# Performance work log

Measured on AMD Instinct MI355X. Metric: run time of the kernel, lower is better.

The kernel has to match this reference:

```python
import jax, jax.numpy as jnp
import numpy as np

B, N, E, H = 8, 512, 256, 8
DK = E // H
DIST_BAR = (0.3, 0.7, 1e10)  # init dist_bar + [1e10] appended in forward
NEG = -1e10


def setup_inputs() -> dict:
    key = jax.random.key(0)
    ks = jax.random.split(key, 24)
    s = 0.02
    inp = {
        'query': jax.random.normal(ks[0], (B, N, E), jnp.float32),
        'key':   jax.random.normal(ks[1], (B, N, E), jnp.float32),
        'value': jax.random.normal(ks[2], (B, N, E), jnp.float32),
        'dist':  jax.random.uniform(ks[3], (B, N, N), jnp.float32),
        'mask':  jax.random.randint(ks[4], (B, N, N), 0, 2).astype(jnp.int32),
        # 4 linears (q, k, v, out), stored as [in, out] for x @ W
        'Wq': jax.random.normal(ks[5], (E, E)) * s, 'bq': jnp.zeros((E,)),
        'Wk': jax.random.normal(ks[6], (E, E)) * s, 'bk': jnp.zeros((E,)),
        'Wv': jax.random.normal(ks[7], (E, E)) * s, 'bv': jnp.zeros((E,)),
        'Wo': jax.random.normal(ks[8], (E, E)) * s, 'bo': jnp.zeros((E,)),
        # cnn: Conv2d(1,H,1) -> ReLU -> Conv2d(H,H,1); 1x1 convs = per-pixel linear maps
        'cw1': jax.random.normal(ks[9], (H,)) * s,     'cb1': jnp.zeros((H,)),
        'cw2': jax.random.normal(ks[10], (H, H)) * s,  'cb2': jnp.zeros((H,)),
        # scale_linear: Linear(3E, E) -> ReLU -> Linear(E, E)
        'Ws1': jax.random.normal(ks[11], (3 * E, E)) * s, 'bs1': jnp.zeros((E,)),
        'Ws2': jax.random.normal(ks[12], (E, E)) * s,     'bs2': jnp.zeros((E,)),
    }
    return inp


def reference(query, key, value, dist, mask,
              Wq, bq, Wk, bk, Wv, bv, Wo, bo,
              cw1, cb1, cw2, cb2, Ws1, bs1, Ws2, bs2):
    def heads(x, W, b):  # [B,N,E] -> [B,H,N,DK]
        return (x @ W + b).reshape(B, N, H, DK).transpose(0, 2, 1, 3)

    q, k, v = heads(query, Wq, bq), heads(key, Wk, bk), heads(value, Wv, bv)
    d4 = dist[:, None]  # [B,1,N,N]
    # 1x1 conv stack: [B,1,N,N] -> [B,H,N,N]
    c1 = jax.nn.relu(d4 * cw1[None, :, None, None] + cb1[None, :, None, None])
    dist_conv = jnp.einsum('oi,bijk->bojk', cw2, c1) + cb2[None, :, None, None]

    scores = jnp.einsum('bhqd,bhkd->bhqk', q, k) / np.sqrt(DK).astype(np.float32)
    scores = scores * dist_conv
    scores = jnp.where(mask[:, None] == 0, NEG, scores)

    outs = []
    for bar in DIST_BAR:
        dm = d4 < bar                       # [B,1,N,N] bool
        dm = dm.at[:, :, 0, :].set(True).at[:, :, :, 0].set(True)
        s = jnp.where(dm, scores, NEG)
        p = jax.nn.softmax(s, axis=-1)      # [B,H,N,N]
        o = jnp.einsum('bhqk,bhkd->bhqd', p, v)
        o = o.transpose(0, 2, 1, 3).reshape(B, N, E)
        outs.append(o @ Wo + bo)
    x = jnp.concatenate(outs, axis=-1)      # [B,N,3E]
    h1 = jax.nn.relu(x @ Ws1 + bs1)
    return h1 @ Ws2 + bs2                   # [B,N,E]
```

## Files before the change

kernel.cpp:

```cpp
#include <hip/hip_runtime.h>
#include <math.h>

typedef _Float16 h16;
typedef __attribute__((ext_vector_type(8))) _Float16 h16x8;
typedef __attribute__((ext_vector_type(4))) float f32x4;
typedef unsigned long long u64t;
typedef unsigned int u32t;
typedef unsigned short u16t;
typedef unsigned char u8t;

__global__ void bcomb_k(const float* __restrict__ bo, const float* __restrict__ Ws1,
                        const float* __restrict__ bs1, float* __restrict__ bcomb)
{
    const int jj = threadIdx.x;
    const int r0 = blockIdx.x * 64;
    float acc = (blockIdx.x == 0) ? bs1[jj] : 0.f;
    for (int r = r0; r < r0 + 64; ++r)
        acc = fmaf(bo[r & 255], Ws1[(size_t)r * 256 + jj], acc);
    atomicAdd(&bcomb[jj], acc);
}

__global__ __launch_bounds__(256) void transpose_k(
    const float* __restrict__ Wq, const float* __restrict__ Wk,
    const float* __restrict__ Wv, const float* __restrict__ Ws2,
    const float* __restrict__ Ws1, h16* __restrict__ WT)
{
    const int z = blockIdx.z;
    const float* in = (z == 0) ? Wq : (z == 1) ? Wk : (z == 2) ? Wv :
                      (z == 3) ? Ws2 : (Ws1 + (size_t)(z - 4) * 65536);
    h16* out = WT + (size_t)z * 65536;
    __shared__ float T[32][33];
    const int t = threadIdx.x, tx = t & 31, ty = t >> 5;
    const int r0 = blockIdx.x * 32, c0 = blockIdx.y * 32;
    #pragma unroll
    for (int i = 0; i < 4; ++i) {
        const int row = ty + i * 8;
        T[row][tx] = in[(size_t)(r0 + row) * 256 + c0 + tx];
    }
    __syncthreads();
    #pragma unroll
    for (int i = 0; i < 4; ++i) {
        const int row = ty + i * 8;
        out[(size_t)(c0 + row) * 256 + r0 + tx] = (h16)T[tx][row];
    }
}

template<int A_F32, int MODE>
__global__ __launch_bounds__(256) void hgemm_k(
    const void* __restrict__ Av, const h16* __restrict__ Bt0,
    const float* __restrict__ bias, void* __restrict__ outv,
    int M, int Nn, int K, long btz, int ldt)
{
    const h16* Bt = Bt0 + (size_t)blockIdx.z * btz;
    __shared__ __align__(16) h16 As[64][40];
    __shared__ __align__(16) h16 Bs[64][40];
    const int t = threadIdx.x, w = t >> 6, lane = t & 63;
    const int Q = lane >> 4, n = lane & 15;
    const int row0 = blockIdx.x * 64, col0 = blockIdx.y * 64;
    const int sr = t >> 2, sc = (t & 3) * 8;
    f32x4 acc[4];
    #pragma unroll
    for (int c = 0; c < 4; ++c) acc[c] = (f32x4){0.f, 0.f, 0.f, 0.f};

    for (int k0 = 0; k0 < K; k0 += 32) {
        __syncthreads();
        if (A_F32) {
            const float* ap = (const float*)Av + (size_t)(row0 + sr) * K + k0 + sc;
            float4 f0 = *(const float4*)ap;
            float4 f1 = *(const float4*)(ap + 4);
            h16x8 hv;
            hv[0] = (h16)f0.x; hv[1] = (h16)f0.y; hv[2] = (h16)f0.z; hv[3] = (h16)f0.w;
            hv[4] = (h16)f1.x; hv[5] = (h16)f1.y; hv[6] = (h16)f1.z; hv[7] = (h16)f1.w;
            *(h16x8*)&As[sr][sc] = hv;
        } else {
            *(h16x8*)&As[sr][sc] =
                *(const h16x8*)((const h16*)Av + (size_t)(row0 + sr) * K + k0 + sc);
        }
        *(h16x8*)&Bs[sr][sc] = *(const h16x8*)(Bt + (size_t)(col0 + sr) * K + k0 + sc);
        __syncthreads();
        h16x8 af = *(const h16x8*)&As[w * 16 + n][Q * 8];
        #pragma unroll
        for (int c = 0; c < 4; ++c) {
            h16x8 bf = *(const h16x8*)&Bs[c * 16 + n][Q * 8];
            acc[c] = __builtin_amdgcn_mfma_f32_16x16x32_f16(af, bf, acc[c], 0, 0, 0);
        }
    }

    float bvv[4] = {0.f, 0.f, 0.f, 0.f};
    if (MODE != 4) {
        #pragma unroll
        for (int c = 0; c < 4; ++c) bvv[c] = bias[col0 + c * 16 + n];
    }
    #pragma unroll
    for (int c = 0; c < 4; ++c) {
        #pragma unroll
        for (int r = 0; r < 4; ++r) {
            const int row = row0 + w * 16 + 4 * Q + r;
            const int col = col0 + c * 16 + n;
            if (MODE == 0) {
                ((float*)outv)[(size_t)row * Nn + col] = acc[c][r] + bvv[c];
            } else if (MODE == 2) {
                ((h16*)outv)[(size_t)row * Nn + col] = (h16)fmaxf(acc[c][r] + bvv[c], 0.f);
            } else {
                ((h16*)outv)[(size_t)col * ldt + (int)blockIdx.z * M + row] = (h16)acc[c][r];
            }
        }
    }
}

__global__ __launch_bounds__(256) void qkv_hgemm_k(
    const float* __restrict__ Xq, const float* __restrict__ Xk,
    const float* __restrict__ Xv, const h16* __restrict__ WT,
    const float* __restrict__ bq, const float* __restrict__ bk,
    const float* __restrict__ bv,
    h16* __restrict__ qb, h16* __restrict__ kb, h16* __restrict__ vbT)
{
    const int z = blockIdx.z;
    const float* A    = (z == 0) ? Xq : (z == 1) ? Xk : Xv;
    const h16*   Bt   = WT + (size_t)z * 65536;
    const float* bias = (z == 0) ? bq : (z == 1) ? bk : bv;

    __shared__ __align__(16) h16 As[64][40];
    __shared__ __align__(16) h16 Bs[64][40];
    const int t = threadIdx.x, w = t >> 6, lane = t & 63;
    const int Q = lane >> 4, n = lane & 15;
    const int row0 = blockIdx.x * 64, col0 = blockIdx.y * 64;
    const int sr = t >> 2, sc = (t & 3) * 8;
    f32x4 acc[4];
    #pragma unroll
    for (int c = 0; c < 4; ++c) acc[c] = (f32x4){0.f, 0.f, 0.f, 0.f};

    for (int k0 = 0; k0 < 256; k0 += 32) {
        __syncthreads();
        {
            const float* ap = A + (size_t)(row0 + sr) * 256 + k0 + sc;
            float4 f0 = *(const float4*)ap;
            float4 f1 = *(const float4*)(ap + 4);
            h16x8 hv;
            hv[0] = (h16)f0.x; hv[1] = (h16)f0.y; hv[2] = (h16)f0.z; hv[3] = (h16)f0.w;
            hv[4] = (h16)f1.x; hv[5] = (h16)f1.y; hv[6] = (h16)f1.z; hv[7] = (h16)f1.w;
            *(h16x8*)&As[sr][sc] = hv;
            *(h16x8*)&Bs[sr][sc] = *(const h16x8*)(Bt + (size_t)(col0 + sr) * 256 + k0 + sc);
        }
        __syncthreads();
        h16x8 af = *(const h16x8*)&As[w * 16 + n][Q * 8];
        #pragma unroll
        for (int c = 0; c < 4; ++c) {
            h16x8 bf = *(const h16x8*)&Bs[c * 16 + n][Q * 8];
            acc[c] = __builtin_amdgcn_mfma_f32_16x16x32_f16(af, bf, acc[c], 0, 0, 0);
        }
    }

    float bvv[4];
    #pragma unroll
    for (int c = 0; c < 4; ++c) bvv[c] = bias[col0 + c * 16 + n];

    if (z < 2) {
        h16* out = z ? kb : qb;
        #pragma unroll
        for (int c = 0; c < 4; ++c)
            #pragma unroll
            for (int r = 0; r < 4; ++r)
                out[(size_t)(row0 + w * 16 + 4 * Q + r) * 256 + col0 + c * 16 + n] =
                    (h16)(acc[c][r] + bvv[c]);
    } else {
        const int bb = row0 >> 9;
        #pragma unroll
        for (int c = 0; c < 4; ++c)
            #pragma unroll
            for (int r = 0; r < 4; ++r) {
                const int m = row0 + w * 16 + 4 * Q + r;
                const int col = col0 + c * 16 + n;
                vbT[((size_t)(bb * 256 + col)) * 512 + (m & 511)] = (h16)(acc[c][r] + bvv[c]);
            }
    }
}

__global__ __launch_bounds__(256, 4) void attn_k(
    const h16* __restrict__ qb, const h16* __restrict__ kb,
    const h16* __restrict__ vbT,
    const float* __restrict__ dist, const int* __restrict__ mask,
    const float* __restrict__ cw1, const float* __restrict__ cb1,
    const float* __restrict__ cw2, const float* __restrict__ cb2,
    h16* __restrict__ OB)
{
    const int bx = blockIdx.x, b = bx >> 5, q0 = (bx & 31) * 16;
    const int t = threadIdx.x, w = t >> 6, lane = t & 63;
    const int Q = lane >> 4, n = lane & 15;
    const int h = blockIdx.y * 4 + w;

    __shared__ __align__(16) h16 c1t[16][65][8];
    __shared__ __align__(16) u8t Cd[16][72];
    __shared__ __align__(16) h16 Sx[4][16][72];

    const float invs = 0.17677669529663687f;
    float w1[8], b1[8], w2w[8];
    #pragma unroll
    for (int u = 0; u < 8; ++u) {
        w1[u] = cw1[u]; b1[u] = cb1[u];
        w2w[u] = invs * cw2[h * 8 + u];
    }
    const float fb = invs * cb2[h];

    const h16x8 aq =
        *(const h16x8*)(qb + ((size_t)(b * 512 + q0 + n)) * 256 + h * 32 + Q * 8);

    const f32x4 z4 = {0.f, 0.f, 0.f, 0.f};
    f32x4 acc[3][2];
    #pragma unroll
    for (int s = 0; s < 3; ++s) { acc[s][0] = z4; acc[s][1] = z4; }
    float mprev = -3e38f;
    float lsum[3] = {0.f, 0.f, 0.f};

    const int scol = t & 63, srow0 = t >> 6;

    for (int kc = 0; kc < 8; ++kc) {
        const int kk0 = kc * 64;
        __syncthreads();
        #pragma unroll
        for (int i = 0; i < 4; ++i) {
            const int row = srow0 + 4 * i;
            const size_t off = ((size_t)(b * 512 + q0 + row)) * 512 + kk0 + scol;
            const float d = dist[off];
            const int mk = mask[off];
            const bool fr = ((q0 + row) == 0) || ((kk0 + scol) == 0);
            const bool keep = (mk != 0);
            const u32t code = (keep && (fr || d < 0.3f) ? 1u : 0u)
                            | (keep && (fr || d < 0.7f) ? 2u : 0u)
                            | (keep ? 4u : 0u);
            Cd[row][scol] = (u8t)code;
            h16x8 ch;
            #pragma unroll
            for (int u = 0; u < 8; ++u)
                ch[u] = (h16)fmaxf(fmaf(d, w1[u], b1[u]), 0.f);
            *(h16x8*)&c1t[row][scol][0] = ch;
        }
        __syncthreads();

        f32x4 s4[4];
        #pragma unroll
        for (int cg = 0; cg < 4; ++cg) {
            h16x8 kf = *(const h16x8*)(
                kb + ((size_t)(b * 512 + kk0 + cg * 16 + n)) * 256 + h * 32 + Q * 8);
            s4[cg] = __builtin_amdgcn_mfma_f32_16x16x32_f16(aq, kf, z4, 0, 0, 0);
        }
        #pragma unroll
        for (int cg = 0; cg < 4; ++cg) {
            #pragma unroll
            for (int r = 0; r < 4; ++r) {
                h16x8 ch = *(const h16x8*)&c1t[4 * Q + r][cg * 16 + n][0];
                float f = fb;
                #pragma unroll
                for (int u = 0; u < 8; ++u)
                    f = fmaf((float)ch[u], w2w[u], f);
                Sx[w][4 * Q + r][cg * 16 + n] = (h16)(s4[cg][r] * f);
            }
        }
        __builtin_amdgcn_wave_barrier();

        float sv[16];
        u64t cd0 = *(const u64t*)&Cd[n][Q * 8];
        u64t cd1 = *(const u64t*)&Cd[n][32 + Q * 8];
        {
            h16x8 sh0 = *(const h16x8*)&Sx[w][n][Q * 8];
            h16x8 sh1 = *(const h16x8*)&Sx[w][n][32 + Q * 8];
            #pragma unroll
            for (int j = 0; j < 8; ++j) { sv[j] = (float)sh0[j]; sv[8 + j] = (float)sh1[j]; }
        }
        float cm = -3e38f;
        #pragma unroll
        for (int i = 0; i < 16; ++i) {
            const u32t cc = (u32t)((i < 8 ? cd0 : cd1) >> (8 * (i & 7))) & 7u;
            cm = fmaxf(cm, (cc & 4u) ? sv[i] : -3e38f);
        }
        cm = fmaxf(cm, __shfl_xor(cm, 16));
        cm = fmaxf(cm, __shfl_xor(cm, 32));
        const float mnew = fmaxf(mprev, cm);
        const float alphaA = __expf(mprev - mnew);
        mprev = mnew;

        #pragma unroll
        for (int r = 0; r < 4; ++r) {
            const float aR = __shfl(alphaA, 4 * Q + r);
            #pragma unroll
            for (int s = 0; s < 3; ++s) { acc[s][0][r] *= aR; acc[s][1][r] *= aR; }
        }

        h16x8 pf[3][2];
        float l0 = 0.f, l1 = 0.f, l2 = 0.f;
        #pragma unroll
        for (int i = 0; i < 16; ++i) {
            const u32t cc = (u32t)((i < 8 ? cd0 : cd1) >> (8 * (i & 7))) & 7u;
            const float e = __expf(sv[i] - mnew);
            const float p0 = (cc & 1u) ? e : 0.f;
            const float p1 = (cc & 2u) ? e : 0.f;
            const float p2 = (cc & 4u) ? e : 0.f;
            l0 += p0; l1 += p1; l2 += p2;
            pf[0][i >> 3][i & 7] = (h16)p0;
            pf[1][i >> 3][i & 7] = (h16)p1;
            pf[2][i >> 3][i & 7] = (h16)p2;
        }
        lsum[0] = lsum[0] * alphaA + l0;
        lsum[1] = lsum[1] * alphaA + l1;
        lsum[2] = lsum[2] * alphaA + l2;

        #pragma unroll
        for (int kb2 = 0; kb2 < 2; ++kb2) {
            #pragma unroll
            for (int nh = 0; nh < 2; ++nh) {
                h16x8 vf = *(const h16x8*)(
                    vbT + ((size_t)((b * 8 + h) * 32 + nh * 16 + n)) * 512
                        + kk0 + kb2 * 32 + Q * 8);
                #pragma unroll
                for (int s = 0; s < 3; ++s)
                    acc[s][nh] = __builtin_amdgcn_mfma_f32_16x16x32_f16(
                        pf[s][kb2], vf, acc[s][nh], 0, 0, 0);
            }
        }
    }

    float lrow[3];
    #pragma unroll
    for (int s = 0; s < 3; ++s) {
        float lv = lsum[s];
        lv += __shfl_xor(lv, 16);
        lv += __shfl_xor(lv, 32);
        lrow[s] = lv;
    }
    #pragma unroll
    for (int s = 0; s < 3; ++s) {
        #pragma unroll
        for (int r = 0; r < 4; ++r) {
            const float il = 1.0f / __shfl(lrow[s], 4 * Q + r);
            const size_t row = (size_t)(b * 512 + q0 + 4 * Q + r);
            h16* op = OB + row * 768 + s * 256 + h * 32 + n;
            op[0]  = (h16)(acc[s][0][r] * il);
            op[16] = (h16)(acc[s][1][r] * il);
        }
    }
}

extern "C" void kernel_launch(void* const* d_in, const int* in_sizes, int n_in,
                              void* d_out, int out_size, void* d_ws, size_t ws_size,
                              hipStream_t stream)
{
    const float* query = (const float*)d_in[0];
    const float* key   = (const float*)d_in[1];
    const float* value = (const float*)d_in[2];
    const float* dist  = (const float*)d_in[3];
    const int*   mask  = (const int*)d_in[4];
    const float* Wq = (const float*)d_in[5];  const float* bq = (const float*)d_in[6];
    const float* Wk = (const float*)d_in[7];  const float* bk = (const float*)d_in[8];
    const float* Wv = (const float*)d_in[9];  const float* bv = (const float*)d_in[10];
    const float* Wo = (const float*)d_in[11]; const float* bo = (const float*)d_in[12];
    const float* cw1 = (const float*)d_in[13]; const float* cb1 = (const float*)d_in[14];
    const float* cw2 = (const float*)d_in[15]; const float* cb2 = (const float*)d_in[16];
    const float* Ws1 = (const float*)d_in[17]; const float* bs1 = (const float*)d_in[18];
    const float* Ws2 = (const float*)d_in[19]; const float* bs2 = (const float*)d_in[20];

    h16* qb    = (h16*)d_ws;
    h16* kb    = qb + 1048576;
    h16* vbT   = kb + 1048576;
    h16* OB    = vbT + 1048576;
    h16* h1    = OB + 3145728;
    h16* WT    = h1 + 1048576;
    h16* WbigT = WT + 458752;
    float* bcomb = (float*)(WbigT + 196608);

    hipMemsetAsync(bcomb, 0, 256 * sizeof(float), stream);
    bcomb_k<<<dim3(12), dim3(256), 0, stream>>>(bo, Ws1, bs1, bcomb);

    transpose_k<<<dim3(8, 8, 7), 256, 0, stream>>>(Wq, Wk, Wv, Ws2, Ws1, WT);

    hgemm_k<1, 4><<<dim3(4, 4, 3), 256, 0, stream>>>(
        Wo, WT + 4 * 65536, nullptr, WbigT, 256, 256, 256, 65536, 768);

    qkv_hgemm_k<<<dim3(64, 4, 3), 256, 0, stream>>>(
        query, key, value, WT, bq, bk, bv, qb, kb, vbT);

    attn_k<<<dim3(256, 2), 256, 0, stream>>>(
        qb, kb, vbT, dist, mask, cw1, cb1, cw2, cb2, OB);

    hgemm_k<0, 2><<<dim3(64, 4, 1), 256, 0, stream>>>(
        OB, WbigT, bcomb, h1, 4096, 256, 768, 0, 0);
    hgemm_k<0, 0><<<dim3(64, 4, 1), 256, 0, stream>>>(
        h1, WT + 3 * 65536, bs2, d_out, 4096, 256, 256, 0, 0);
}
```

Baseline: 193.2 us.

## Fuse prep kernels, double-buffer GEMMs and prefetch attention tiles

Merges the weight-transpose and bias-combination kernels into one launch and folds the Wo weight-combination GEMM into the QKV projection launch, which drops the memset and several launches. All GEMMs now double-buffer shared memory with register prefetch, and the tail GEMMs use 32-row tiles with K-step 64 so they launch more blocks. Attention precomputes the per-head conv factor during staging and prefetches the next chunk's dist/mask/K/V into registers. It lowers attention occupancy to 2 blocks per SM to make room for the extra registers.

```diff
diff --git a/kernel.cpp b/kernel.cpp
--- a/kernel.cpp
+++ b/kernel.cpp
@@ -6,177 +6,225 @@
 typedef __attribute__((ext_vector_type(4))) float f32x4;
 typedef unsigned long long u64t;
 typedef unsigned int u32t;
-typedef unsigned short u16t;
 typedef unsigned char u8t;
 
-__global__ void bcomb_k(const float* __restrict__ bo, const float* __restrict__ Ws1,
-                        const float* __restrict__ bs1, float* __restrict__ bcomb)
-{
-    const int jj = threadIdx.x;
-    const int r0 = blockIdx.x * 64;
-    float acc = (blockIdx.x == 0) ? bs1[jj] : 0.f;
-    for (int r = r0; r < r0 + 64; ++r)
-        acc = fmaf(bo[r & 255], Ws1[(size_t)r * 256 + jj], acc);
-    atomicAdd(&bcomb[jj], acc);
-}
-
-__global__ __launch_bounds__(256) void transpose_k(
+__global__ __launch_bounds__(256) void prep_k(
     const float* __restrict__ Wq, const float* __restrict__ Wk,
     const float* __restrict__ Wv, const float* __restrict__ Ws2,
-    const float* __restrict__ Ws1, h16* __restrict__ WT)
+    const float* __restrict__ Ws1, const float* __restrict__ bo,
+    const float* __restrict__ bs1, h16* __restrict__ WT,
+    float* __restrict__ bcomb)
 {
-    const int z = blockIdx.z;
-    const float* in = (z == 0) ? Wq : (z == 1) ? Wk : (z == 2) ? Wv :
-                      (z == 3) ? Ws2 : (Ws1 + (size_t)(z - 4) * 65536);
-    h16* out = WT + (size_t)z * 65536;
+    const int bid = blockIdx.x;
     __shared__ float T[32][33];
-    const int t = threadIdx.x, tx = t & 31, ty = t >> 5;
-    const int r0 = blockIdx.x * 32, c0 = blockIdx.y * 32;
-    #pragma unroll
-    for (int i = 0; i < 4; ++i) {
-        const int row = ty + i * 8;
-        T[row][tx] = in[(size_t)(r0 + row) * 256 + c0 + tx];
-    }
-    __syncthreads();
-    #pragma unroll
-    for (int i = 0; i < 4; ++i) {
-        const int row = ty + i * 8;
-        out[(size_t)(c0 + row) * 256 + r0 + tx] = (h16)T[tx][row];
+    if (bid < 448) {
+        const int z = bid >> 6, idx = bid & 63;
+        const float* in = (z == 0) ? Wq : (z == 1) ? Wk : (z == 2) ? Wv :
+                          (z == 3) ? Ws2 : (Ws1 + (size_t)(z - 4) * 65536);
+        h16* out = WT + (size_t)z * 65536;
+        const int t = threadIdx.x, tx = t & 31, ty = t >> 5;
+        const int r0 = (idx >> 3) * 32, c0 = (idx & 7) * 32;
+        #pragma unroll
+        for (int i = 0; i < 4; ++i)
+            T[ty + i * 8][tx] = in[(size_t)(r0 + ty + i * 8) * 256 + c0 + tx];
+        __syncthreads();
+        #pragma unroll
+        for (int i = 0; i < 4; ++i)
+            out[(size_t)(c0 + ty + i * 8) * 256 + r0 + tx] = (h16)T[tx][ty + i * 8];
+    } else {
+        const int j = threadIdx.x;
+        float acc = bs1[j];
+        for (int r = 0; r < 768; ++r)
+            acc = fmaf(bo[r & 255], Ws1[(size_t)r * 256 + j], acc);
+        bcomb[j] = acc;
     }
 }
 
-template<int A_F32, int MODE>
-__global__ __launch_bounds__(256) void hgemm_k(
-    const void* __restrict__ Av, const h16* __restrict__ Bt0,
-    const float* __restrict__ bias, void* __restrict__ outv,
-    int M, int Nn, int K, long btz, int ldt)
+__global__ __launch_bounds__(256) void qkvw_k(
+    const float* __restrict__ Xq, const float* __restrict__ Xk,
+    const float* __restrict__ Xv, const float* __restrict__ Wo,
+    const h16* __restrict__ WT,
+    const float* __restrict__ bq, const float* __restrict__ bk,
+    const float* __restrict__ bv,
+    h16* __restrict__ qb, h16* __restrict__ kb, h16* __restrict__ vbT,
+    h16* __restrict__ WbigT)
 {
-    const h16* Bt = Bt0 + (size_t)blockIdx.z * btz;
-    __shared__ __align__(16) h16 As[64][40];
-    __shared__ __align__(16) h16 Bs[64][40];
+    const int bid = blockIdx.x;
+    const float* A; const h16* Bt; const float* bias = nullptr;
+    int mode, row0, col0, sgm = 0;
+    if (bid < 768) {
+        const int z = bid >> 8, r = bid & 255;
+        row0 = (r & 63) * 64; col0 = (r >> 6) * 64;
+        A = (z == 0) ? Xq : (z == 1) ? Xk : Xv;
+        Bt = WT + (size_t)z * 65536;
+        bias = (z == 0) ? bq : (z == 1) ? bk : bv;
+        mode = z;
+    } else {
+        const int r = bid - 768;
+        sgm = r >> 4; const int tt = r & 15;
+        row0 = (tt >> 2) * 64; col0 = (tt & 3) * 64;
+        A = Wo; Bt = WT + (size_t)(4 + sgm) * 65536; mode = 3;
+    }
+
+    __shared__ __align__(16) h16 As[2][64][40];
+    __shared__ __align__(16) h16 Bs[2][64][40];
     const int t = threadIdx.x, w = t >> 6, lane = t & 63;
     const int Q = lane >> 4, n = lane & 15;
-    const int row0 = blockIdx.x * 64, col0 = blockIdx.y * 64;
     const int sr = t >> 2, sc = (t & 3) * 8;
-    f32x4 acc[4];
-    #pragma unroll
-    for (int c = 0; c < 4; ++c) acc[c] = (f32x4){0.f, 0.f, 0.f, 0.f};
-
-    for (int k0 = 0; k0 < K; k0 += 32) {
+
+    auto ldA = [&](int k0) -> h16x8 {
+        const float* ap = A + (size_t)(row0 + sr) * 256 + k0 + sc;
+        float4 f0 = *(const float4*)ap;
+        float4 f1 = *(const float4*)(ap + 4);
+        h16x8 hv;
+        hv[0] = (h16)f0.x; hv[1] = (h16)f0.y; hv[2] = (h16)f0.z; hv[3] = (h16)f0.w;
+        hv[4] = (h16)f1.x; hv[5] = (h16)f1.y; hv[6] = (h16)f1.z; hv[7] = (h16)f1.w;
+        return hv;
+    };
+    auto ldB = [&](int k0) -> h16x8 {
+        return *(const h16x8*)(Bt + (size_t)(col0 + sr) * 256 + k0 + sc);
+    };
+
+    {
+        h16x8 a0 = ldA(0), b0 = ldB(0);
+        *(h16x8*)&As[0][sr][sc] = a0;
+        *(h16x8*)&Bs[0][sr][sc] = b0;
+    }
+    __syncthreads();
+
+    f32x4 acc4[4];
+    #pragma unroll
+    for (int c = 0; c < 4; ++c) acc4[c] = (f32x4){0.f, 0.f, 0.f, 0.f};
+
+    for (int it = 0; it < 8; ++it) {
+        const int cur = it & 1;
+        h16x8 arN, brN;
+        if (it < 7) { arN = ldA(32 * (it + 1)); brN = ldB(32 * (it + 1)); }
+        h16x8 af = *(const h16x8*)&As[cur][w * 16 + n][Q * 8];
+        #pragma unroll
+        for (int cg = 0; cg < 4; ++cg) {
+            h16x8 bf = *(const h16x8*)&Bs[cur][cg * 16 + n][Q * 8];
+            acc4[cg] = __builtin_amdgcn_mfma_f32_16x16x32_f16(af, bf, acc4[cg], 0, 0, 0);
+        }
+        if (it < 7) {
+            *(h16x8*)&As[cur ^ 1][sr][sc] = arN;
+            *(h16x8*)&Bs[cur ^ 1][sr][sc] = brN;
+        }
         __syncthreads();
-        if (A_F32) {
-            const float* ap = (const float*)Av + (size_t)(row0 + sr) * K + k0 + sc;
-            float4 f0 = *(const float4*)ap;
-            float4 f1 = *(const float4*)(ap + 4);
-            h16x8 hv;
-            hv[0] = (h16)f0.x; hv[1] = (h16)f0.y; hv[2] = (h16)f0.z; hv[3] = (h16)f0.w;
-            hv[4] = (h16)f1.x; hv[5] = (h16)f1.y; hv[6] = (h16)f1.z; hv[7] = (h16)f1.w;
-            *(h16x8*)&As[sr][sc] = hv;
-        } else {
-            *(h16x8*)&As[sr][sc] =
-                *(const h16x8*)((const h16*)Av + (size_t)(row0 + sr) * K + k0 + sc);
-        }
-        *(h16x8*)&Bs[sr][sc] = *(const h16x8*)(Bt + (size_t)(col0 + sr) * K + k0 + sc);
-        __syncthreads();
-        h16x8 af = *(const h16x8*)&As[w * 16 + n][Q * 8];
-        #pragma unroll
-        for (int c = 0; c < 4; ++c) {
-            h16x8 bf = *(const h16x8*)&Bs[c * 16 + n][Q * 8];
-            acc[c] = __builtin_amdgcn_mfma_f32_16x16x32_f16(af, bf, acc[c], 0, 0, 0);
-        }
-    }
-
-    float bvv[4] = {0.f, 0.f, 0.f, 0.f};
-    if (MODE != 4) {
-        #pragma unroll
-        for (int c = 0; c < 4; ++c) bvv[c] = bias[col0 + c * 16 + n];
-    }
-    #pragma unroll
-    for (int c = 0; c < 4; ++c) {
-        #pragma unroll
-        for (int r = 0; r < 4; ++r) {
-            const int row = row0 + w * 16 + 4 * Q + r;
-            const int col = col0 + c * 16 + n;
-            if (MODE == 0) {
-                ((float*)outv)[(size_t)row * Nn + col] = acc[c][r] + bvv[c];
-            } else if (MODE == 2) {
-                ((h16*)outv)[(size_t)row * Nn + col] = (h16)fmaxf(acc[c][r] + bvv[c], 0.f);
-            } else {
-                ((h16*)outv)[(size_t)col * ldt + (int)blockIdx.z * M + row] = (h16)acc[c][r];
+    }
+
+    if (mode < 2) {
+        h16* out = mode ? kb : qb;
+        #pragma unroll
+        for (int cg = 0; cg < 4; ++cg) {
+            const float bvv = bias[col0 + cg * 16 + n];
+            #pragma unroll
+            for (int r = 0; r < 4; ++r)
+                out[(size_t)(row0 + w * 16 + 4 * Q + r) * 256 + col0 + cg * 16 + n] =
+                    (h16)(acc4[cg][r] + bvv);
+        }
+    } else if (mode == 2) {
+        const int bb = row0 >> 9;
+        #pragma unroll
+        for (int cg = 0; cg < 4; ++cg) {
+            const float bvv = bias[col0 + cg * 16 + n];
+            const int col = col0 + cg * 16 + n;
+            #pragma unroll
+            for (int r = 0; r < 4; ++r) {
+                const int m = row0 + w * 16 + 4 * Q + r;
+                vbT[((size_t)(bb * 256 + col)) * 512 + (m & 511)] = (h16)(acc4[cg][r] + bvv);
             }
         }
+    } else {
+        #pragma unroll
+        for (int cg = 0; cg < 4; ++cg) {
+            const int col = col0 + cg * 16 + n;
+            #pragma unroll
+            for (int r = 0; r < 4; ++r)
+                WbigT[(size_t)col * 768 + sgm * 256 + row0 + w * 16 + 4 * Q + r] =
+                    (h16)acc4[cg][r];
+        }
     }
 }
 
-__global__ __launch_bounds__(256) void qkv_hgemm_k(
-    const float* __restrict__ Xq, const float* __restrict__ Xk,
-    const float* __restrict__ Xv, const h16* __restrict__ WT,
-    const float* __restrict__ bq, const float* __restrict__ bk,
-    const float* __restrict__ bv,
-    h16* __restrict__ qb, h16* __restrict__ kb, h16* __restrict__ vbT)
+template<int OUT16RELU>
+__global__ __launch_bounds__(256) void hgemm32_k(
+    const h16* __restrict__ A, const h16* __restrict__ Bt,
+    const float* __restrict__ bias, void* __restrict__ outv, int K)
 {
-    const int z = blockIdx.z;
-    const float* A    = (z == 0) ? Xq : (z == 1) ? Xk : Xv;
-    const h16*   Bt   = WT + (size_t)z * 65536;
-    const float* bias = (z == 0) ? bq : (z == 1) ? bk : bv;
-
-    __shared__ __align__(16) h16 As[64][40];
-    __shared__ __align__(16) h16 Bs[64][40];
+    __shared__ __align__(16) h16 As[2][32][72];
+    __shared__ __align__(16) h16 Bs[2][64][72];
     const int t = threadIdx.x, w = t >> 6, lane = t & 63;
     const int Q = lane >> 4, n = lane & 15;
-    const int row0 = blockIdx.x * 64, col0 = blockIdx.y * 64;
-    const int sr = t >> 2, sc = (t & 3) * 8;
-    f32x4 acc[4];
-    #pragma unroll
-    for (int c = 0; c < 4; ++c) acc[c] = (f32x4){0.f, 0.f, 0.f, 0.f};
-
-    for (int k0 = 0; k0 < 256; k0 += 32) {
+    const int row0 = blockIdx.x * 32, col0 = blockIdx.y * 64;
+    const int r16 = (w & 1) * 16, c32 = (w >> 1) * 32;
+    const int asr = t >> 3, asc = (t & 7) * 8;
+    const int bsr = t >> 2, bsc = (t & 3) * 16;
+
+    auto ldA = [&](int k0) -> h16x8 {
+        return *(const h16x8*)(A + (size_t)(row0 + asr) * K + k0 + asc);
+    };
+    auto ldB0 = [&](int k0) -> h16x8 {
+        return *(const h16x8*)(Bt + (size_t)(col0 + bsr) * K + k0 + bsc);
+    };
+    auto ldB1 = [&](int k0) -> h16x8 {
+        return *(const h16x8*)(Bt + (size_t)(col0 + bsr) * K + k0 + bsc + 8);
+    };
+
+    {
+        h16x8 a0 = ldA(0), b0 = ldB0(0), b1 = ldB1(0);
+        *(h16x8*)&As[0][asr][asc] = a0;
+        *(h16x8*)&Bs[0][bsr][bsc] = b0;
+        *(h16x8*)&Bs[0][bsr][bsc + 8] = b1;
+    }
+    __syncthreads();
+
+    f32x4 acc2[2];
+    acc2[0] = (f32x4){0.f, 0.f, 0.f, 0.f};
+    acc2[1] = (f32x4){0.f, 0.f, 0.f, 0.f};
+    const int iters = K >> 6;
+
+    for (int it = 0; it < iters; ++it) {
+        const int cur = it & 1;
+        h16x8 arN, brN0, brN1;
+        if (it + 1 < iters) {
+            arN = ldA(64 * (it + 1));
+            brN0 = ldB0(64 * (it + 1));
+            brN1 = ldB1(64 * (it + 1));
+        }
+        #pragma unroll
+        for (int kh = 0; kh < 2; ++kh) {
+            h16x8 af = *(const h16x8*)&As[cur][r16 + n][kh * 32 + Q * 8];
+            #pragma unroll
+            for (int cg = 0; cg < 2; ++cg) {
+                h16x8 bf = *(const h16x8*)&Bs[cur][c32 + cg * 16 + n][kh * 32 + Q * 8];
+                acc2[cg] = __builtin_amdgcn_mfma_f32_16x16x32_f16(af, bf, acc2[cg], 0, 0, 0);
+            }
+        }
+        if (it + 1 < iters) {
+            *(h16x8*)&As[cur ^ 1][asr][asc] = arN;
+            *(h16x8*)&Bs[cur ^ 1][bsr][bsc] = brN0;
+            *(h16x8*)&Bs[cur ^ 1][bsr][bsc + 8] = brN1;
+        }
         __syncthreads();
-        {
-            const float* ap = A + (size_t)(row0 + sr) * 256 + k0 + sc;
-            float4 f0 = *(const float4*)ap;
-            float4 f1 = *(const float4*)(ap + 4);
-            h16x8 hv;
-            hv[0] = (h16)f0.x; hv[1] = (h16)f0.y; hv[2] = (h16)f0.z; hv[3] = (h16)f0.w;
-            hv[4] = (h16)f1.x; hv[5] = (h16)f1.y; hv[6] = (h16)f1.z; hv[7] = (h16)f1.w;
-            *(h16x8*)&As[sr][sc] = hv;
-            *(h16x8*)&Bs[sr][sc] = *(const h16x8*)(Bt + (size_t)(col0 + sr) * 256 + k0 + sc);
-        }
-        __syncthreads();
-        h16x8 af = *(const h16x8*)&As[w * 16 + n][Q * 8];
-        #pragma unroll
-        for (int c = 0; c < 4; ++c) {
-            h16x8 bf = *(const h16x8*)&Bs[c * 16 + n][Q * 8];
-            acc[c] = __builtin_amdgcn_mfma_f32_16x16x32_f16(af, bf, acc[c], 0, 0, 0);
-        }
-    }
-
-    float bvv[4];
-    #pragma unroll
-    for (int c = 0; c < 4; ++c) bvv[c] = bias[col0 + c * 16 + n];
-
-    if (z < 2) {
-        h16* out = z ? kb : qb;
-        #pragma unroll
-        for (int c = 0; c < 4; ++c)
-            #pragma unroll
-            for (int r = 0; r < 4; ++r)
-                out[(size_t)(row0 + w * 16 + 4 * Q + r) * 256 + col0 + c * 16 + n] =
-                    (h16)(acc[c][r] + bvv[c]);
-    } else {
-        const int bb = row0 >> 9;
-        #pragma unroll
-        for (int c = 0; c < 4; ++c)
-            #pragma unroll
-            for (int r = 0; r < 4; ++r) {
-                const int m = row0 + w * 16 + 4 * Q + r;
-                const int col = col0 + c * 16 + n;
-                vbT[((size_t)(bb * 256 + col)) * 512 + (m & 511)] = (h16)(acc[c][r] + bvv[c]);
-            }
+    }
+
+    #pragma unroll
+    for (int cg = 0; cg < 2; ++cg) {
+        const int col = col0 + c32 + cg * 16 + n;
+        const float bv = bias[col];
+        #pragma unroll
+        for (int r = 0; r < 4; ++r) {
+            const int row = row0 + r16 + 4 * Q + r;
+            if (OUT16RELU)
+                ((h16*)outv)[(size_t)row * 256 + col] = (h16)fmaxf(acc2[cg][r] + bv, 0.f);
+            else
+                ((float*)outv)[(size_t)row * 256 + col] = acc2[cg][r] + bv;
+        }
     }
 }
 
-__global__ __launch_bounds__(256, 4) void attn_k(
+__global__ __launch_bounds__(256, 2) void attn_k(
     const h16* __restrict__ qb, const h16* __restrict__ kb,
     const h16* __restrict__ vbT,
     const float* __restrict__ dist, const int* __restrict__ mask,
@@ -185,22 +233,26 @@
     h16* __restrict__ OB)
 {
     const int bx = blockIdx.x, b = bx >> 5, q0 = (bx & 31) * 16;
+    const int hg = blockIdx.y;
     const int t = threadIdx.x, w = t >> 6, lane = t & 63;
     const int Q = lane >> 4, n = lane & 15;
-    const int h = blockIdx.y * 4 + w;
-
-    __shared__ __align__(16) h16 c1t[16][65][8];
-    __shared__ __align__(16) u8t Cd[16][72];
+    const int h = hg * 4 + w;
+
+    __shared__ __align__(16) h16 Ft[2][4][16][68];
+    __shared__ __align__(16) u8t Cd[2][16][72];
     __shared__ __align__(16) h16 Sx[4][16][72];
 
     const float invs = 0.17677669529663687f;
-    float w1[8], b1[8], w2w[8];
-    #pragma unroll
-    for (int u = 0; u < 8; ++u) {
-        w1[u] = cw1[u]; b1[u] = cb1[u];
-        w2w[u] = invs * cw2[h * 8 + u];
-    }
-    const float fb = invs * cb2[h];
+    float w1[8], b1[8];
+    #pragma unroll
+    for (int u = 0; u < 8; ++u) { w1[u] = cw1[u]; b1[u] = cb1[u]; }
+    float w2a[4][8], fba[4];
+    #pragma unroll
+    for (int hh = 0; hh < 4; ++hh) {
+        #pragma unroll
+        for (int u = 0; u < 8; ++u) w2a[hh][u] = invs * cw2[(hg * 4 + hh) * 8 + u];
+        fba[hh] = invs * cb2[hg * 4 + hh];
+    }
 
     const h16x8 aq =
         *(const h16x8*)(qb + ((size_t)(b * 512 + q0 + n)) * 256 + h * 32 + Q * 8);
@@ -212,60 +264,97 @@
     float mprev = -3e38f;
     float lsum[3] = {0.f, 0.f, 0.f};
 
-    const int scol = t & 63, srow0 = t >> 6;
-
-    for (int kc = 0; kc < 8; ++kc) {
-        const int kk0 = kc * 64;
-        __syncthreads();
+    const int scol = lane;
+
+    auto stage = [&](int buf, int kkb, const float* dp, const int* mp) {
         #pragma unroll
         for (int i = 0; i < 4; ++i) {
-            const int row = srow0 + 4 * i;
-            const size_t off = ((size_t)(b * 512 + q0 + row)) * 512 + kk0 + scol;
-            const float d = dist[off];
-            const int mk = mask[off];
-            const bool fr = ((q0 + row) == 0) || ((kk0 + scol) == 0);
-            const bool keep = (mk != 0);
+            const int row = w + 4 * i;
+            const float d = dp[i];
+            const bool fr = ((q0 + row) == 0) || ((kkb + scol) == 0);
+            const bool keep = (mp[i] != 0);
             const u32t code = (keep && (fr || d < 0.3f) ? 1u : 0u)
                             | (keep && (fr || d < 0.7f) ? 2u : 0u)
                             | (keep ? 4u : 0u);
-            Cd[row][scol] = (u8t)code;
-            h16x8 ch;
-            #pragma unroll
-            for (int u = 0; u < 8; ++u)
-                ch[u] = (h16)fmaxf(fmaf(d, w1[u], b1[u]), 0.f);
-            *(h16x8*)&c1t[row][scol][0] = ch;
-        }
-        __syncthreads();
+            Cd[buf][row][scol] = (u8t)code;
+            float ch[8];
+            #pragma unroll
+            for (int u = 0; u < 8; ++u) ch[u] = fmaxf(fmaf(d, w1[u], b1[u]), 0.f);
+            #pragma unroll
+            for (int hh = 0; hh < 4; ++hh) {
+                float f = fba[hh];
+                #pragma unroll
+                for (int u = 0; u < 8; ++u) f = fmaf(ch[u], w2a[hh][u], f);
+                Ft[buf][hh][row][scol] = (h16)f;
+            }
+        }
+    };
+
+    float dv[4]; int mkv[4];
+    #pragma unroll
+    for (int i = 0; i < 4; ++i) {
+        const size_t off = ((size_t)(b * 512 + q0 + w + 4 * i)) * 512 + scol;
+        dv[i] = dist[off]; mkv[i] = mask[off];
+    }
+    h16x8 kf[4], vf[4];
+    #pragma unroll
+    for (int cg = 0; cg < 4; ++cg)
+        kf[cg] = *(const h16x8*)(kb + ((size_t)(b * 512 + cg * 16 + n)) * 256 + h * 32 + Q * 8);
+    #pragma unroll
+    for (int nh = 0; nh < 2; ++nh)
+        #pragma unroll
+        for (int k2 = 0; k2 < 2; ++k2)
+            vf[nh * 2 + k2] = *(const h16x8*)(
+                vbT + ((size_t)((b * 8 + h) * 32 + nh * 16 + n)) * 512 + k2 * 32 + Q * 8);
+    stage(0, 0, dv, mkv);
+    __syncthreads();
+
+    for (int kc = 0; kc < 8; ++kc) {
+        const int cur = kc & 1, kk0 = kc * 64;
+
+        float dN[4]; int mkN[4]; h16x8 kfN[4], vfN[4];
+        if (kc < 7) {
+            const int kn = kk0 + 64;
+            #pragma unroll
+            for (int i = 0; i < 4; ++i) {
+                const size_t off = ((size_t)(b * 512 + q0 + w + 4 * i)) * 512 + kn + scol;
+                dN[i] = dist[off]; mkN[i] = mask[off];
+            }
+            #pragma unroll
+            for (int cg = 0; cg < 4; ++cg)
+                kfN[cg] = *(const h16x8*)(
+                    kb + ((size_t)(b * 512 + kn + cg * 16 + n)) * 256 + h * 32 + Q * 8);
+            #pragma unroll
+            for (int nh = 0; nh < 2; ++nh)
+                #pragma unroll
+                for (int k2 = 0; k2 < 2; ++k2)
+                    vfN[nh * 2 + k2] = *(const h16x8*)(
+                        vbT + ((size_t)((b * 8 + h) * 32 + nh * 16 + n)) * 512
+                            + kn + k2 * 32 + Q * 8);
+        }
 
         f32x4 s4[4];
         #pragma unroll
-        for (int cg = 0; cg < 4; ++cg) {
-            h16x8 kf = *(const h16x8*)(
-                kb + ((size_t)(b * 512 + kk0 + cg * 16 + n)) * 256 + h * 32 + Q * 8);
-            s4[cg] = __builtin_amdgcn_mfma_f32_16x16x32_f16(aq, kf, z4, 0, 0, 0);
-        }
-        #pragma unroll
-        for (int cg = 0; cg < 4; ++cg) {
+        for (int cg = 0; cg < 4; ++cg)
+            s4[cg] = __builtin_amdgcn_mfma_f32_16x16x32_f16(aq, kf[cg], z4, 0, 0, 0);
+
+        #pragma unroll
+        for (int cg = 0; cg < 4; ++cg)
             #pragma unroll
             for (int r = 0; r < 4; ++r) {
-                h16x8 ch = *(const h16x8*)&c1t[4 * Q + r][cg * 16 + n][0];
-                float f = fb;
-                #pragma unroll
-                for (int u = 0; u < 8; ++u)
-                    f = fmaf((float)ch[u], w2w[u], f);
+                const float f = (float)Ft[cur][w][4 * Q + r][cg * 16 + n];
                 Sx[w][4 * Q + r][cg * 16 + n] = (h16)(s4[cg][r] * f);
             }
-        }
         __builtin_amdgcn_wave_barrier();
 
+        const u64t cd0 = *(const u64t*)&Cd[cur][n][Q * 8];
+        const u64t cd1 = *(const u64t*)&Cd[cur][n][32 + Q * 8];
         float sv[16];
-        u64t cd0 = *(const u64t*)&Cd[n][Q * 8];
-        u64t cd1 = *(const u64t*)&Cd[n][32 + Q * 8];
         {
-            h16x8 sh0 = *(const h16x8*)&Sx[w][n][Q * 8];
-            h16x8 sh1 = *(const h16x8*)&Sx[w][n][32 + Q * 8];
-            #pragma unroll
-            for (int j = 0; j < 8; ++j) { sv[j] = (float)sh0[j]; sv[8 + j] = (float)sh1[j]; }
+            h16x8 s0 = *(const h16x8*)&Sx[w][n][Q * 8];
+            h16x8 s1 = *(const h16x8*)&Sx[w][n][32 + Q * 8];
+            #pragma unroll
+            for (int j = 0; j < 8; ++j) { sv[j] = (float)s0[j]; sv[8 + j] = (float)s1[j]; }
         }
         float cm = -3e38f;
         #pragma unroll
@@ -305,18 +394,20 @@
         lsum[2] = lsum[2] * alphaA + l2;
 
         #pragma unroll
-        for (int kb2 = 0; kb2 < 2; ++kb2) {
-            #pragma unroll
-            for (int nh = 0; nh < 2; ++nh) {
-                h16x8 vf = *(const h16x8*)(
-                    vbT + ((size_t)((b * 8 + h) * 32 + nh * 16 + n)) * 512
-                        + kk0 + kb2 * 32 + Q * 8);
+        for (int k2 = 0; k2 < 2; ++k2)
+            #pragma unroll
+            for (int nh = 0; nh < 2; ++nh)
                 #pragma unroll
                 for (int s = 0; s < 3; ++s)
                     acc[s][nh] = __builtin_amdgcn_mfma_f32_16x16x32_f16(
-                        pf[s][kb2], vf, acc[s][nh], 0, 0, 0);
-            }
-        }
+                        pf[s][k2], vf[nh * 2 + k2], acc[s][nh], 0, 0, 0);
+
+        if (kc < 7) {
+            stage(cur ^ 1, kk0 + 64, dN, mkN);
+            #pragma unroll
+            for (int i = 0; i < 4; ++i) { kf[i] = kfN[i]; vf[i] = vfN[i]; dv[i] = dN[i]; mkv[i] = mkN[i]; }
+        }
+        __syncthreads();
     }
 
     float lrow[3];
@@ -367,22 +458,14 @@
     h16* WbigT = WT + 458752;
     float* bcomb = (float*)(WbigT + 196608);
 
-    hipMemsetAsync(bcomb, 0, 256 * sizeof(float), stream);
-    bcomb_k<<<dim3(12), dim3(256), 0, stream>>>(bo, Ws1, bs1, bcomb);
-
-    transpose_k<<<dim3(8, 8, 7), 256, 0, stream>>>(Wq, Wk, Wv, Ws2, Ws1, WT);
-
-    hgemm_k<1, 4><<<dim3(4, 4, 3), 256, 0, stream>>>(
-        Wo, WT + 4 * 65536, nullptr, WbigT, 256, 256, 256, 65536, 768);
-
-    qkv_hgemm_k<<<dim3(64, 4, 3), 256, 0, stream>>>(
-        query, key, value, WT, bq, bk, bv, qb, kb, vbT);
-
-    attn_k<<<dim3(256, 2), 256, 0, stream>>>(
-        qb, kb, vbT, dist, mask, cw1, cb1, cw2, cb2, OB);
-
-    hgemm_k<0, 2><<<dim3(64, 4, 1), 256, 0, stream>>>(
-        OB, WbigT, bcomb, h1, 4096, 256, 768, 0, 0);
-    hgemm_k<0, 0><<<dim3(64, 4, 1), 256, 0, stream>>>(
-        h1, WT + 3 * 65536, bs2, d_out, 4096, 256, 256, 0, 0);
+    prep_k<<<dim3(449), 256, 0, stream>>>(Wq, Wk, Wv, Ws2, Ws1, bo, bs1, WT, bcomb);
+
+    qkvw_k<<<dim3(816), 256, 0, stream>>>(query, key, value, Wo, WT,
+                                          bq, bk, bv, qb, kb, vbT, WbigT);
+
+    attn_k<<<dim3(256, 2), 256, 0, stream>>>(qb, kb, vbT, dist, mask,
+                                             cw1, cb1, cw2, cb2, OB);
+
+    hgemm32_k<1><<<dim3(128, 4), 256, 0, stream>>>(OB, WbigT, bcomb, h1, 768);
+    hgemm32_k<0><<<dim3(128, 4), 256, 0, stream>>>(h1, WT + 3 * 65536, bs2, d_out, 256);
 }
```

After: 187.0 us. -3.2%, faster.
